# Kernel optimization log

Hardware: AMD Instinct MI355X
Metric: run time of the kernel (lower is better)

Reference implementation:

```python
import jax, jax.numpy as jnp
import numpy as np

BATCH = 16      # self.batch_size
EPS = 1e-5      # BatchNorm2d default eps


def setup_inputs() -> dict:
    key = jax.random.key(0)
    ks = jax.random.split(key, 8)
    inp = {
        # mailbox['agg_feat']: [total_nodes = B*npoints, K, C_in] = [16384, 64, 67]
        'agg_feat': jax.random.normal(ks[0], (16384, 64, 67), jnp.float32),
        # layer 0: Conv2d(67, 64, 1) + BN(64)
        'w0': jax.random.normal(ks[1], (64, 67), jnp.float32) * 0.1,
        'b0': jnp.zeros((64,), jnp.float32),
        'g0': jnp.ones((64,), jnp.float32),
        'be0': jnp.zeros((64,), jnp.float32),
        # layer 1: Conv2d(64, 64, 1) + BN(64)
        'w1': jax.random.normal(ks[2], (64, 64), jnp.float32) * 0.1,
        'b1': jnp.zeros((64,), jnp.float32),
        'g1': jnp.ones((64,), jnp.float32),
        'be1': jnp.zeros((64,), jnp.float32),
        # layer 2: Conv2d(64, 128, 1) + BN(128)
        'w2': jax.random.normal(ks[3], (128, 64), jnp.float32) * 0.1,
        'b2': jnp.zeros((128,), jnp.float32),
        'g2': jnp.ones((128,), jnp.float32),
        'be2': jnp.zeros((128,), jnp.float32),
    }
    return inp


def _conv_bn_relu(h, w, b, g, be):
    # 1x1 Conv2d on NCHW: contraction over input channels only
    h = jnp.einsum('oc,bcnk->bonk', w, h) + b[None, :, None, None]
    # BatchNorm2d in training mode: biased batch stats over (B, N, K) per channel
    mean = jnp.mean(h, axis=(0, 2, 3), keepdims=True)
    var = jnp.mean(jnp.square(h - mean), axis=(0, 2, 3), keepdims=True)
    h = (h - mean) * jax.lax.rsqrt(var + EPS)
    h = h * g[None, :, None, None] + be[None, :, None, None]
    return jax.nn.relu(h)


def reference(agg_feat, w0, b0, g0, be0, w1, b1, g1, be1, w2, b2, g2, be2):
    total, K, C = agg_feat.shape
    npoints = total // BATCH
    # [total, K, C] -> [B, npoints, K, C] -> [B, C, npoints, K]
    h = agg_feat.reshape(BATCH, npoints, K, C).transpose(0, 3, 1, 2)
    for w, b, g, be in ((w0, b0, g0, be0), (w1, b1, g1, be1), (w2, b2, g2, be2)):
        h = _conv_bn_relu(h, w, b, g, be)
    # max over neighbor axis K -> [B, C_out, npoints]
    h = jnp.max(h, axis=3)
    feat_dim = h.shape[1]
    # [B, C_out, npoints] -> [B, npoints, C_out] -> [B*npoints, C_out]
    return h.transpose(0, 2, 1).reshape(-1, feat_dim)
```

## Files before the change

kernel.cpp:

```cpp
#include <hip/hip_runtime.h>

#define ROWS  16384
#define PTOT  1048576
#define NTOTF 1048576.0f
#define EPSF  1e-5f
#define NREP  16

typedef _Float16 half8  __attribute__((ext_vector_type(8)));
typedef _Float16 half2v __attribute__((ext_vector_type(2)));
typedef __fp16   fp16x2 __attribute__((ext_vector_type(2)));
typedef __attribute__((ext_vector_type(4))) float floatx4;
typedef float f32x4 __attribute__((ext_vector_type(4)));
typedef f32x4 f32x4u __attribute__((aligned(4)));

union H8 { half8 v8; half2v v2[4]; };
union PK2 { fp16x2 p; half2v h; unsigned int u; };

__device__ __forceinline__ half2v cvt2(float lo, float hi) {
    PK2 k; k.p = __builtin_amdgcn_cvt_pkrtz(lo, hi); return k.h;
}
__device__ __forceinline__ unsigned int cvt2u(float lo, float hi) {
    PK2 k; k.p = __builtin_amdgcn_cvt_pkrtz(lo, hi); return k.u;
}
__device__ __forceinline__ float relu_f(float x) { return x > 0.f ? x : 0.f; }

__device__ __forceinline__ half8 h8zero() {
    half8 z = {(_Float16)0.f, (_Float16)0.f, (_Float16)0.f, (_Float16)0.f,
               (_Float16)0.f, (_Float16)0.f, (_Float16)0.f, (_Float16)0.f};
    return z;
}

__device__ __forceinline__ half2v bn2(half2v h, half2v a, half2v b) {
    half2v z = {(_Float16)0.f, (_Float16)0.f};
    return __builtin_elementwise_max((half2v)(h * a + b), z);
}

__global__ __launch_bounds__(256) void k_conv0(
    const float* __restrict__ X, const float* __restrict__ w0,
    const float* __restrict__ b0, _Float16* __restrict__ H,
    float* __restrict__ stats)
{
    __shared__ float sred[64], s2red[64];
    const int tid  = threadIdx.x;
    const int lane = tid & 63;
    const int wid  = tid >> 6;
    const int ln15 = lane & 15;
    const int quad = lane >> 4;
    const int pbase = blockIdx.x * 256 + wid * 64;

    if (tid < 64) { sred[tid] = 0.f; s2red[tid] = 0.f; }
    __syncthreads();

    half8 afr[4][3];
    floatx4 bias[4];
#pragma unroll
    for (int mt = 0; mt < 4; ++mt) {
        const float* wr = w0 + (size_t)(mt * 16 + ln15) * 67;
#pragma unroll
        for (int kh = 0; kh < 2; ++kh) {
            f32x4u wa = *reinterpret_cast<const f32x4u*>(wr + kh * 32 + quad * 8);
            f32x4u wb = *reinterpret_cast<const f32x4u*>(wr + kh * 32 + quad * 8 + 4);
            H8 t;
            t.v2[0] = cvt2(wa[0], wa[1]);
            t.v2[1] = cvt2(wa[2], wa[3]);
            t.v2[2] = cvt2(wb[0], wb[1]);
            t.v2[3] = cvt2(wb[2], wb[3]);
            afr[mt][kh] = t.v8;
        }
        H8 t; t.v8 = h8zero();
        if (quad == 0) {
            f32x4u tv = *reinterpret_cast<const f32x4u*>(wr + 63);
            t.v2[0] = cvt2(tv[1], tv[2]);
            t.v2[1] = cvt2(tv[3], 0.f);
        }
        afr[mt][2] = t.v8;
        bias[mt] = *reinterpret_cast<const floatx4*>(b0 + mt * 16 + quad * 4);
    }

    float s[4][4] = {}, s2[4][4] = {};
#pragma unroll 2
    for (int nt = 0; nt < 4; ++nt) {
        const int pos = pbase + nt * 16 + ln15;
        const float* xr = X + (size_t)pos * 67;
        H8 B0, B1, BT;
        {
            f32x4u xa = *reinterpret_cast<const f32x4u*>(xr + quad * 8);
            f32x4u xb = *reinterpret_cast<const f32x4u*>(xr + quad * 8 + 4);
            f32x4u xc = *reinterpret_cast<const f32x4u*>(xr + 32 + quad * 8);
            f32x4u xd = *reinterpret_cast<const f32x4u*>(xr + 32 + quad * 8 + 4);
            B0.v2[0] = cvt2(xa[0], xa[1]);
            B0.v2[1] = cvt2(xa[2], xa[3]);
            B0.v2[2] = cvt2(xb[0], xb[1]);
            B0.v2[3] = cvt2(xb[2], xb[3]);
            B1.v2[0] = cvt2(xc[0], xc[1]);
            B1.v2[1] = cvt2(xc[2], xc[3]);
            B1.v2[2] = cvt2(xd[0], xd[1]);
            B1.v2[3] = cvt2(xd[2], xd[3]);
            BT.v8 = h8zero();
            if (quad == 0) {
                f32x4u tv = *reinterpret_cast<const f32x4u*>(xr + 63);
                BT.v2[0] = cvt2(tv[1], tv[2]);
                BT.v2[1] = cvt2(tv[3], 0.f);
            }
        }
#pragma unroll
        for (int mt = 0; mt < 4; ++mt) {
            floatx4 c = bias[mt];
            c = __builtin_amdgcn_mfma_f32_16x16x32_f16(afr[mt][0], B0.v8, c, 0, 0, 0);
            c = __builtin_amdgcn_mfma_f32_16x16x32_f16(afr[mt][1], B1.v8, c, 0, 0, 0);
            c = __builtin_amdgcn_mfma_f32_16x16x32_f16(afr[mt][2], BT.v8, c, 0, 0, 0);
            s[mt][0] += c[0]; s2[mt][0] += c[0] * c[0];
            s[mt][1] += c[1]; s2[mt][1] += c[1] * c[1];
            s[mt][2] += c[2]; s2[mt][2] += c[2] * c[2];
            s[mt][3] += c[3]; s2[mt][3] += c[3] * c[3];
            uint2 o;
            o.x = cvt2u(c[0], c[1]);
            o.y = cvt2u(c[2], c[3]);
            *reinterpret_cast<uint2*>(&H[(size_t)pos * 64 + mt * 16 + quad * 4]) = o;
        }
    }
#pragma unroll
    for (int mt = 0; mt < 4; ++mt)
#pragma unroll
        for (int rg = 0; rg < 4; ++rg) {
            s[mt][rg]  += __shfl_xor(s[mt][rg], 1, 64);  s[mt][rg]  += __shfl_xor(s[mt][rg], 2, 64);
            s[mt][rg]  += __shfl_xor(s[mt][rg], 4, 64);  s[mt][rg]  += __shfl_xor(s[mt][rg], 8, 64);
            s2[mt][rg] += __shfl_xor(s2[mt][rg], 1, 64); s2[mt][rg] += __shfl_xor(s2[mt][rg], 2, 64);
            s2[mt][rg] += __shfl_xor(s2[mt][rg], 4, 64); s2[mt][rg] += __shfl_xor(s2[mt][rg], 8, 64);
        }
    if (ln15 == 0) {
#pragma unroll
        for (int mt = 0; mt < 4; ++mt)
#pragma unroll
            for (int rg = 0; rg < 4; ++rg) {
                atomicAdd(&sred[mt * 16 + quad * 4 + rg], s[mt][rg]);
                atomicAdd(&s2red[mt * 16 + quad * 4 + rg], s2[mt][rg]);
            }
    }
    __syncthreads();
    const int rep = (blockIdx.x & (NREP - 1)) * 512;
    if (tid < 64) {
        unsafeAtomicAdd(&stats[rep + tid], sred[tid]);
        unsafeAtomicAdd(&stats[rep + 64 + tid], s2red[tid]);
    }
}

__global__ __launch_bounds__(256) void k_conv1(
    const _Float16* __restrict__ Hin, _Float16* __restrict__ Hout,
    const float* __restrict__ w1, const float* __restrict__ b1,
    const float* __restrict__ g0, const float* __restrict__ be0,
    float* __restrict__ stats)
{
    __shared__ float als[64], bls[64], sred[64], s2red[64];
    const int tid  = threadIdx.x;
    const int lane = tid & 63;
    const int wid  = tid >> 6;
    const int ln15 = lane & 15;
    const int quad = lane >> 4;
    const int pbase = blockIdx.x * 256 + wid * 64;

    if (tid < 64) {
        float ssum = 0.f, qsum = 0.f;
#pragma unroll
        for (int r = 0; r < NREP; ++r) { ssum += stats[r * 512 + tid]; qsum += stats[r * 512 + 64 + tid]; }
        const float mean = ssum * (1.f / NTOTF);
        const float var  = qsum * (1.f / NTOTF) - mean * mean;
        const float a    = g0[tid] / sqrtf(var + EPSF);
        als[tid] = a; bls[tid] = be0[tid] - mean * a;
        sred[tid] = 0.f; s2red[tid] = 0.f;
    }
    __syncthreads();

    half2v a2[8], b2[8];
#pragma unroll
    for (int kh = 0; kh < 2; ++kh)
#pragma unroll
        for (int j2 = 0; j2 < 4; ++j2) {
            const int c0 = kh * 32 + quad * 8 + 2 * j2;
            half2v av = {(_Float16)als[c0], (_Float16)als[c0 + 1]};
            half2v bv = {(_Float16)bls[c0], (_Float16)bls[c0 + 1]};
            a2[kh * 4 + j2] = av; b2[kh * 4 + j2] = bv;
        }

    half8 afr[4][2];
    floatx4 bias[4];
#pragma unroll
    for (int mt = 0; mt < 4; ++mt) {
        const float* wr = w1 + (size_t)(mt * 16 + ln15) * 64;
#pragma unroll
        for (int kh = 0; kh < 2; ++kh) {
            f32x4 wa = *reinterpret_cast<const f32x4*>(wr + kh * 32 + quad * 8);
            f32x4 wb = *reinterpret_cast<const f32x4*>(wr + kh * 32 + quad * 8 + 4);
            H8 t;
            t.v2[0] = cvt2(wa[0], wa[1]);
            t.v2[1] = cvt2(wa[2], wa[3]);
            t.v2[2] = cvt2(wb[0], wb[1]);
            t.v2[3] = cvt2(wb[2], wb[3]);
            afr[mt][kh] = t.v8;
        }
        bias[mt] = *reinterpret_cast<const floatx4*>(b1 + mt * 16 + quad * 4);
    }

    float s[4][4] = {}, s2[4][4] = {};
#pragma unroll 2
    for (int nt = 0; nt < 4; ++nt) {
        const int pos = pbase + nt * 16 + ln15;
        H8 r0, r1;
        r0.v8 = *reinterpret_cast<const half8*>(&Hin[(size_t)pos * 64 + quad * 8]);
        r1.v8 = *reinterpret_cast<const half8*>(&Hin[(size_t)pos * 64 + 32 + quad * 8]);
        H8 f0, f1;
#pragma unroll
        for (int j2 = 0; j2 < 4; ++j2) {
            f0.v2[j2] = bn2(r0.v2[j2], a2[j2], b2[j2]);
            f1.v2[j2] = bn2(r1.v2[j2], a2[4 + j2], b2[4 + j2]);
        }
#pragma unroll
        for (int mt = 0; mt < 4; ++mt) {
            floatx4 c = bias[mt];
            c = __builtin_amdgcn_mfma_f32_16x16x32_f16(afr[mt][0], f0.v8, c, 0, 0, 0);
            c = __builtin_amdgcn_mfma_f32_16x16x32_f16(afr[mt][1], f1.v8, c, 0, 0, 0);
            s[mt][0] += c[0]; s2[mt][0] += c[0] * c[0];
            s[mt][1] += c[1]; s2[mt][1] += c[1] * c[1];
            s[mt][2] += c[2]; s2[mt][2] += c[2] * c[2];
            s[mt][3] += c[3]; s2[mt][3] += c[3] * c[3];
            uint2 o;
            o.x = cvt2u(c[0], c[1]);
            o.y = cvt2u(c[2], c[3]);
            *reinterpret_cast<uint2*>(&Hout[(size_t)pos * 64 + mt * 16 + quad * 4]) = o;
        }
    }
#pragma unroll
    for (int mt = 0; mt < 4; ++mt)
#pragma unroll
        for (int rg = 0; rg < 4; ++rg) {
            s[mt][rg]  += __shfl_xor(s[mt][rg], 1, 64);  s[mt][rg]  += __shfl_xor(s[mt][rg], 2, 64);
            s[mt][rg]  += __shfl_xor(s[mt][rg], 4, 64);  s[mt][rg]  += __shfl_xor(s[mt][rg], 8, 64);
            s2[mt][rg] += __shfl_xor(s2[mt][rg], 1, 64); s2[mt][rg] += __shfl_xor(s2[mt][rg], 2, 64);
            s2[mt][rg] += __shfl_xor(s2[mt][rg], 4, 64); s2[mt][rg] += __shfl_xor(s2[mt][rg], 8, 64);
        }
    if (ln15 == 0) {
#pragma unroll
        for (int mt = 0; mt < 4; ++mt)
#pragma unroll
            for (int rg = 0; rg < 4; ++rg) {
                atomicAdd(&sred[mt * 16 + quad * 4 + rg], s[mt][rg]);
                atomicAdd(&s2red[mt * 16 + quad * 4 + rg], s2[mt][rg]);
            }
    }
    __syncthreads();
    const int rep = (blockIdx.x & (NREP - 1)) * 512;
    if (tid < 64) {
        unsafeAtomicAdd(&stats[rep + 128 + tid], sred[tid]);
        unsafeAtomicAdd(&stats[rep + 192 + tid], s2red[tid]);
    }
}

__global__ __launch_bounds__(256) void k_conv2(
    const _Float16* __restrict__ H, const float* __restrict__ w2,
    const float* __restrict__ b2c, const float* __restrict__ g1,
    const float* __restrict__ be1, float* __restrict__ rowmax,
    float* __restrict__ rowmin, float* __restrict__ stats)
{
    __shared__ float als[64], bls[64], sred[128], s2red[128];
    const int tid  = threadIdx.x;
    const int lane = tid & 63;
    const int wid  = tid >> 6;
    const int ln15 = lane & 15;
    const int quad = lane >> 4;
    const int r0   = blockIdx.x * 4;

    if (tid < 64) {
        float ssum = 0.f, qsum = 0.f;
#pragma unroll
        for (int r = 0; r < NREP; ++r) { ssum += stats[r * 512 + 128 + tid]; qsum += stats[r * 512 + 192 + tid]; }
        const float mean = ssum * (1.f / NTOTF);
        const float var  = qsum * (1.f / NTOTF) - mean * mean;
        const float a    = g1[tid] / sqrtf(var + EPSF);
        als[tid] = a; bls[tid] = be1[tid] - mean * a;
    }
    if (tid < 128) { sred[tid] = 0.f; s2red[tid] = 0.f; }
    __syncthreads();

    half2v a2[8], b2[8];
#pragma unroll
    for (int kh = 0; kh < 2; ++kh)
#pragma unroll
        for (int j2 = 0; j2 < 4; ++j2) {
            const int c0 = kh * 32 + quad * 8 + 2 * j2;
            half2v av = {(_Float16)als[c0], (_Float16)als[c0 + 1]};
            half2v bv = {(_Float16)bls[c0], (_Float16)bls[c0 + 1]};
            a2[kh * 4 + j2] = av; b2[kh * 4 + j2] = bv;
        }

    const int chHalf = (wid & 1) * 64;
    half8 bfr[8];
    float biasn[4];
#pragma unroll
    for (int nt = 0; nt < 4; ++nt) {
        const int n = chHalf + nt * 16 + ln15;
        biasn[nt] = b2c[n];
#pragma unroll
        for (int kh = 0; kh < 2; ++kh) {
            f32x4 wa = *reinterpret_cast<const f32x4*>(&w2[(size_t)n * 64 + kh * 32 + quad * 8]);
            f32x4 wb = *reinterpret_cast<const f32x4*>(&w2[(size_t)n * 64 + kh * 32 + quad * 8 + 4]);
            H8 t;
            t.v2[0] = cvt2(wa[0], wa[1]);
            t.v2[1] = cvt2(wa[2], wa[3]);
            t.v2[2] = cvt2(wb[0], wb[1]);
            t.v2[3] = cvt2(wb[2], wb[3]);
            bfr[nt * 2 + kh] = t.v8;
        }
    }

    float s[4] = {0, 0, 0, 0}, s2[4] = {0, 0, 0, 0};
    for (int rr = 0; rr < 2; ++rr) {
        const int prow = r0 + (wid >> 1) * 2 + rr;
        float mx[4] = {-3.4e38f, -3.4e38f, -3.4e38f, -3.4e38f};
        float mn[4] = {3.4e38f, 3.4e38f, 3.4e38f, 3.4e38f};
#pragma unroll 2
        for (int mt = 0; mt < 4; ++mt) {
            const size_t rowb = (size_t)(prow * 64 + mt * 16 + ln15) * 64;
            H8 r0f, r1f;
            r0f.v8 = *reinterpret_cast<const half8*>(&H[rowb + quad * 8]);
            r1f.v8 = *reinterpret_cast<const half8*>(&H[rowb + 32 + quad * 8]);
            H8 f0, f1;
#pragma unroll
            for (int j2 = 0; j2 < 4; ++j2) {
                f0.v2[j2] = bn2(r0f.v2[j2], a2[j2], b2[j2]);
                f1.v2[j2] = bn2(r1f.v2[j2], a2[4 + j2], b2[4 + j2]);
            }
#pragma unroll
            for (int nt = 0; nt < 4; ++nt) {
                floatx4 a = {biasn[nt], biasn[nt], biasn[nt], biasn[nt]};
                a = __builtin_amdgcn_mfma_f32_16x16x32_f16(f0.v8, bfr[nt * 2 + 0], a, 0, 0, 0);
                a = __builtin_amdgcn_mfma_f32_16x16x32_f16(f1.v8, bfr[nt * 2 + 1], a, 0, 0, 0);
#pragma unroll
                for (int rg = 0; rg < 4; ++rg) {
                    const float h = a[rg];
                    mx[nt] = fmaxf(mx[nt], h);
                    mn[nt] = fminf(mn[nt], h);
                    s[nt] += h; s2[nt] += h * h;
                }
            }
        }
#pragma unroll
        for (int nt = 0; nt < 4; ++nt) {
            mx[nt] = fmaxf(mx[nt], __shfl_xor(mx[nt], 16, 64));
            mx[nt] = fmaxf(mx[nt], __shfl_xor(mx[nt], 32, 64));
            mn[nt] = fminf(mn[nt], __shfl_xor(mn[nt], 16, 64));
            mn[nt] = fminf(mn[nt], __shfl_xor(mn[nt], 32, 64));
        }
        if (lane < 16) {
#pragma unroll
            for (int nt = 0; nt < 4; ++nt) {
                rowmax[(size_t)prow * 128 + chHalf + nt * 16 + lane] = mx[nt];
                rowmin[(size_t)prow * 128 + chHalf + nt * 16 + lane] = mn[nt];
            }
        }
    }
#pragma unroll
    for (int nt = 0; nt < 4; ++nt) {
        s[nt]  += __shfl_xor(s[nt], 16, 64);  s[nt]  += __shfl_xor(s[nt], 32, 64);
        s2[nt] += __shfl_xor(s2[nt], 16, 64); s2[nt] += __shfl_xor(s2[nt], 32, 64);
    }
    if (lane < 16) {
#pragma unroll
        for (int nt = 0; nt < 4; ++nt) {
            atomicAdd(&sred[chHalf + nt * 16 + ln15], s[nt]);
            atomicAdd(&s2red[chHalf + nt * 16 + ln15], s2[nt]);
        }
    }
    __syncthreads();
    const int rep = (blockIdx.x & (NREP - 1)) * 512;
    if (tid < 128) {
        unsafeAtomicAdd(&stats[rep + 256 + tid], sred[tid]);
        unsafeAtomicAdd(&stats[rep + 384 + tid], s2red[tid]);
    }
}

__global__ __launch_bounds__(256) void k_out(
    const float* __restrict__ rowmax, const float* __restrict__ rowmin,
    const float* __restrict__ g2, const float* __restrict__ be2,
    const float* __restrict__ stats, float* __restrict__ out)
{
    __shared__ float als[128], bls[128];
    const int tid = threadIdx.x;
    if (tid < 128) {
        float ssum = 0.f, qsum = 0.f;
#pragma unroll
        for (int r = 0; r < NREP; ++r) { ssum += stats[r * 512 + 256 + tid]; qsum += stats[r * 512 + 384 + tid]; }
        const float mean = ssum * (1.f / NTOTF);
        const float var  = qsum * (1.f / NTOTF) - mean * mean;
        const float a    = g2[tid] / sqrtf(var + EPSF);
        als[tid] = a; bls[tid] = be2[tid] - mean * a;
    }
    __syncthreads();
    const int idx = blockIdx.x * 256 + tid;
    const int o = idx & 127;
    const float a = als[o];
    const float v = (a > 0.f) ? rowmax[idx] : rowmin[idx];
    out[idx] = relu_f(a * v + bls[o]);
}

extern "C" void kernel_launch(void* const* d_in, const int* in_sizes, int n_in,
                              void* d_out, int out_size, void* d_ws, size_t ws_size,
                              hipStream_t stream)
{
    (void)in_sizes; (void)n_in; (void)out_size; (void)ws_size;
    const float* X   = (const float*)d_in[0];
    const float* w0  = (const float*)d_in[1];
    const float* b0  = (const float*)d_in[2];
    const float* g0  = (const float*)d_in[3];
    const float* be0 = (const float*)d_in[4];
    const float* w1  = (const float*)d_in[5];
    const float* b1  = (const float*)d_in[6];
    const float* g1  = (const float*)d_in[7];
    const float* be1 = (const float*)d_in[8];
    const float* w2  = (const float*)d_in[9];
    const float* b2  = (const float*)d_in[10];
    const float* g2  = (const float*)d_in[11];
    const float* be2 = (const float*)d_in[12];
    float* out = (float*)d_out;

    char* ws = (char*)d_ws;
    _Float16* H = (_Float16*)ws;
    float* rowmax = (float*)(ws + 134217728);
    float* rowmin = (float*)(ws + 134217728 + 8388608);
    float* stats  = (float*)(ws + 134217728 + 2 * 8388608);

    hipMemsetAsync(stats, 0, NREP * 512 * sizeof(float), stream);
    hipLaunchKernelGGL(k_conv0, dim3(PTOT / 256), dim3(256), 0, stream, X, w0, b0, H, stats);
    hipLaunchKernelGGL(k_conv1, dim3(PTOT / 256), dim3(256), 0, stream, H, H, w1, b1, g0, be0, stats);
    hipLaunchKernelGGL(k_conv2, dim3(ROWS / 4), dim3(256), 0, stream, H, w2, b2, g1, be1, rowmax, rowmin, stats);
    hipLaunchKernelGGL(k_out, dim3(ROWS * 128 / 256), dim3(256), 0, stream, rowmax, rowmin, g2, be2, stats, out);
}
```

Measured before the change: 600.1 us.

## Fuse all conv/BN stages into one persistent kernel with grid barriers

Replaces the four separate launches with a single persistent kernel of 512 blocks that loops over its slice of points and uses software grid barriers (atomic counter plus flag) between the batch-norm statistics phases. The per-row max/min of the last layer stay in shared memory, and the final BN+ReLU output is written directly, so the rowmax/rowmin global round trip and the extra launches go away. In exchange, the design relies on all 512 blocks being co-resident (launch_bounds 256,2) to avoid deadlock, carries about 33KB of shared memory per block, and may lose latency hiding because each block does more serial work.

```diff
diff --git a/kernel.cpp b/kernel.cpp
--- a/kernel.cpp
+++ b/kernel.cpp
@@ -5,6 +5,7 @@
 #define NTOTF 1048576.0f
 #define EPSF  1e-5f
 #define NREP  16
+#define NBLK  512
 
 typedef _Float16 half8  __attribute__((ext_vector_type(8)));
 typedef _Float16 half2v __attribute__((ext_vector_type(2)));
@@ -35,134 +36,156 @@
     return __builtin_elementwise_max((half2v)(h * a + b), z);
 }
 
-__global__ __launch_bounds__(256) void k_conv0(
-    const float* __restrict__ X, const float* __restrict__ w0,
-    const float* __restrict__ b0, _Float16* __restrict__ H,
-    float* __restrict__ stats)
+__device__ __forceinline__ float aload(const float* p) {
+    return __hip_atomic_load(p, __ATOMIC_RELAXED, __HIP_MEMORY_SCOPE_AGENT);
+}
+
+__device__ __forceinline__ void gridbar(unsigned int* cnt, unsigned int* flg) {
+    __syncthreads();
+    if (threadIdx.x == 0) {
+        __threadfence();
+        if (atomicAdd(cnt, 1u) == NBLK - 1u) {
+            __threadfence();
+            __hip_atomic_store(flg, 1u, __ATOMIC_RELEASE, __HIP_MEMORY_SCOPE_AGENT);
+        } else {
+            while (__hip_atomic_load(flg, __ATOMIC_ACQUIRE, __HIP_MEMORY_SCOPE_AGENT) == 0u)
+                __builtin_amdgcn_s_sleep(8);
+        }
+    }
+    __syncthreads();
+}
+
+__global__ __launch_bounds__(256, 2) void k_fused(
+    const float* __restrict__ X,
+    const float* __restrict__ w0, const float* __restrict__ b0,
+    const float* __restrict__ g0, const float* __restrict__ be0,
+    const float* __restrict__ w1, const float* __restrict__ b1,
+    const float* __restrict__ g1, const float* __restrict__ be1,
+    const float* __restrict__ w2, const float* __restrict__ cb2,
+    const float* __restrict__ g2, const float* __restrict__ be2,
+    const _Float16* __restrict__ Hin, _Float16* __restrict__ Hout,
+    float* __restrict__ stats, unsigned int* __restrict__ bar,
+    float* __restrict__ out)
 {
-    __shared__ float sred[64], s2red[64];
+    __shared__ float als[128], bls[128], sred[128], s2red[128];
+    __shared__ float smx[32 * 128], smn[32 * 128];
+
     const int tid  = threadIdx.x;
     const int lane = tid & 63;
     const int wid  = tid >> 6;
     const int ln15 = lane & 15;
     const int quad = lane >> 4;
-    const int pbase = blockIdx.x * 256 + wid * 64;
+    const int blk  = blockIdx.x;
+    const int rep  = (blk & (NREP - 1)) * 512;
 
     if (tid < 64) { sred[tid] = 0.f; s2red[tid] = 0.f; }
     __syncthreads();
 
-    half8 afr[4][3];
-    floatx4 bias[4];
-#pragma unroll
-    for (int mt = 0; mt < 4; ++mt) {
-        const float* wr = w0 + (size_t)(mt * 16 + ln15) * 67;
-#pragma unroll
-        for (int kh = 0; kh < 2; ++kh) {
-            f32x4u wa = *reinterpret_cast<const f32x4u*>(wr + kh * 32 + quad * 8);
-            f32x4u wb = *reinterpret_cast<const f32x4u*>(wr + kh * 32 + quad * 8 + 4);
-            H8 t;
-            t.v2[0] = cvt2(wa[0], wa[1]);
-            t.v2[1] = cvt2(wa[2], wa[3]);
-            t.v2[2] = cvt2(wb[0], wb[1]);
-            t.v2[3] = cvt2(wb[2], wb[3]);
-            afr[mt][kh] = t.v8;
-        }
-        H8 t; t.v8 = h8zero();
-        if (quad == 0) {
-            f32x4u tv = *reinterpret_cast<const f32x4u*>(wr + 63);
-            t.v2[0] = cvt2(tv[1], tv[2]);
-            t.v2[1] = cvt2(tv[3], 0.f);
-        }
-        afr[mt][2] = t.v8;
-        bias[mt] = *reinterpret_cast<const floatx4*>(b0 + mt * 16 + quad * 4);
-    }
-
-    float s[4][4] = {}, s2[4][4] = {};
+    {
+        half8 afr[4][3];
+        floatx4 bias[4];
+#pragma unroll
+        for (int mt = 0; mt < 4; ++mt) {
+            const float* wr = w0 + (size_t)(mt * 16 + ln15) * 67;
+#pragma unroll
+            for (int kh = 0; kh < 2; ++kh) {
+                f32x4u wa = *reinterpret_cast<const f32x4u*>(wr + kh * 32 + quad * 8);
+                f32x4u wb = *reinterpret_cast<const f32x4u*>(wr + kh * 32 + quad * 8 + 4);
+                H8 t;
+                t.v2[0] = cvt2(wa[0], wa[1]);
+                t.v2[1] = cvt2(wa[2], wa[3]);
+                t.v2[2] = cvt2(wb[0], wb[1]);
+                t.v2[3] = cvt2(wb[2], wb[3]);
+                afr[mt][kh] = t.v8;
+            }
+            H8 t; t.v8 = h8zero();
+            if (quad == 0) {
+                f32x4u tv = *reinterpret_cast<const f32x4u*>(wr + 63);
+                t.v2[0] = cvt2(tv[1], tv[2]);
+                t.v2[1] = cvt2(tv[3], 0.f);
+            }
+            afr[mt][2] = t.v8;
+            bias[mt] = *reinterpret_cast<const floatx4*>(b0 + mt * 16 + quad * 4);
+        }
+
+        float s[4][4] = {}, s2[4][4] = {};
+        for (int it = 0; it < 8; ++it) {
+            const int pbase = blk * 2048 + it * 256 + wid * 64;
 #pragma unroll 2
-    for (int nt = 0; nt < 4; ++nt) {
-        const int pos = pbase + nt * 16 + ln15;
-        const float* xr = X + (size_t)pos * 67;
-        H8 B0, B1, BT;
-        {
-            f32x4u xa = *reinterpret_cast<const f32x4u*>(xr + quad * 8);
-            f32x4u xb = *reinterpret_cast<const f32x4u*>(xr + quad * 8 + 4);
-            f32x4u xc = *reinterpret_cast<const f32x4u*>(xr + 32 + quad * 8);
-            f32x4u xd = *reinterpret_cast<const f32x4u*>(xr + 32 + quad * 8 + 4);
-            B0.v2[0] = cvt2(xa[0], xa[1]);
-            B0.v2[1] = cvt2(xa[2], xa[3]);
-            B0.v2[2] = cvt2(xb[0], xb[1]);
-            B0.v2[3] = cvt2(xb[2], xb[3]);
-            B1.v2[0] = cvt2(xc[0], xc[1]);
-            B1.v2[1] = cvt2(xc[2], xc[3]);
-            B1.v2[2] = cvt2(xd[0], xd[1]);
-            B1.v2[3] = cvt2(xd[2], xd[3]);
-            BT.v8 = h8zero();
-            if (quad == 0) {
-                f32x4u tv = *reinterpret_cast<const f32x4u*>(xr + 63);
-                BT.v2[0] = cvt2(tv[1], tv[2]);
-                BT.v2[1] = cvt2(tv[3], 0.f);
-            }
-        }
-#pragma unroll
-        for (int mt = 0; mt < 4; ++mt) {
-            floatx4 c = bias[mt];
-            c = __builtin_amdgcn_mfma_f32_16x16x32_f16(afr[mt][0], B0.v8, c, 0, 0, 0);
-            c = __builtin_amdgcn_mfma_f32_16x16x32_f16(afr[mt][1], B1.v8, c, 0, 0, 0);
-            c = __builtin_amdgcn_mfma_f32_16x16x32_f16(afr[mt][2], BT.v8, c, 0, 0, 0);
-            s[mt][0] += c[0]; s2[mt][0] += c[0] * c[0];
-            s[mt][1] += c[1]; s2[mt][1] += c[1] * c[1];
-            s[mt][2] += c[2]; s2[mt][2] += c[2] * c[2];
-            s[mt][3] += c[3]; s2[mt][3] += c[3] * c[3];
-            uint2 o;
-            o.x = cvt2u(c[0], c[1]);
-            o.y = cvt2u(c[2], c[3]);
-            *reinterpret_cast<uint2*>(&H[(size_t)pos * 64 + mt * 16 + quad * 4]) = o;
-        }
-    }
-#pragma unroll
-    for (int mt = 0; mt < 4; ++mt)
-#pragma unroll
-        for (int rg = 0; rg < 4; ++rg) {
-            s[mt][rg]  += __shfl_xor(s[mt][rg], 1, 64);  s[mt][rg]  += __shfl_xor(s[mt][rg], 2, 64);
-            s[mt][rg]  += __shfl_xor(s[mt][rg], 4, 64);  s[mt][rg]  += __shfl_xor(s[mt][rg], 8, 64);
-            s2[mt][rg] += __shfl_xor(s2[mt][rg], 1, 64); s2[mt][rg] += __shfl_xor(s2[mt][rg], 2, 64);
-            s2[mt][rg] += __shfl_xor(s2[mt][rg], 4, 64); s2[mt][rg] += __shfl_xor(s2[mt][rg], 8, 64);
-        }
-    if (ln15 == 0) {
+            for (int nt = 0; nt < 4; ++nt) {
+                const int pos = pbase + nt * 16 + ln15;
+                const float* xr = X + (size_t)pos * 67;
+                H8 B0, B1, BT;
+                {
+                    f32x4u xa = *reinterpret_cast<const f32x4u*>(xr + quad * 8);
+                    f32x4u xb = *reinterpret_cast<const f32x4u*>(xr + quad * 8 + 4);
+                    f32x4u xc = *reinterpret_cast<const f32x4u*>(xr + 32 + quad * 8);
+                    f32x4u xd = *reinterpret_cast<const f32x4u*>(xr + 32 + quad * 8 + 4);
+                    B0.v2[0] = cvt2(xa[0], xa[1]);
+                    B0.v2[1] = cvt2(xa[2], xa[3]);
+                    B0.v2[2] = cvt2(xb[0], xb[1]);
+                    B0.v2[3] = cvt2(xb[2], xb[3]);
+                    B1.v2[0] = cvt2(xc[0], xc[1]);
+                    B1.v2[1] = cvt2(xc[2], xc[3]);
+                    B1.v2[2] = cvt2(xd[0], xd[1]);
+                    B1.v2[3] = cvt2(xd[2], xd[3]);
+                    BT.v8 = h8zero();
+                    if (quad == 0) {
+                        f32x4u tv = *reinterpret_cast<const f32x4u*>(xr + 63);
+                        BT.v2[0] = cvt2(tv[1], tv[2]);
+                        BT.v2[1] = cvt2(tv[3], 0.f);
+                    }
+                }
+#pragma unroll
+                for (int mt = 0; mt < 4; ++mt) {
+                    floatx4 c = bias[mt];
+                    c = __builtin_amdgcn_mfma_f32_16x16x32_f16(afr[mt][0], B0.v8, c, 0, 0, 0);
+                    c = __builtin_amdgcn_mfma_f32_16x16x32_f16(afr[mt][1], B1.v8, c, 0, 0, 0);
+                    c = __builtin_amdgcn_mfma_f32_16x16x32_f16(afr[mt][2], BT.v8, c, 0, 0, 0);
+                    s[mt][0] += c[0]; s2[mt][0] += c[0] * c[0];
+                    s[mt][1] += c[1]; s2[mt][1] += c[1] * c[1];
+                    s[mt][2] += c[2]; s2[mt][2] += c[2] * c[2];
+                    s[mt][3] += c[3]; s2[mt][3] += c[3] * c[3];
+                    uint2 o;
+                    o.x = cvt2u(c[0], c[1]);
+                    o.y = cvt2u(c[2], c[3]);
+                    *reinterpret_cast<uint2*>(&Hout[(size_t)pos * 64 + mt * 16 + quad * 4]) = o;
+                }
+            }
+        }
 #pragma unroll
         for (int mt = 0; mt < 4; ++mt)
 #pragma unroll
             for (int rg = 0; rg < 4; ++rg) {
-                atomicAdd(&sred[mt * 16 + quad * 4 + rg], s[mt][rg]);
-                atomicAdd(&s2red[mt * 16 + quad * 4 + rg], s2[mt][rg]);
-            }
-    }
-    __syncthreads();
-    const int rep = (blockIdx.x & (NREP - 1)) * 512;
-    if (tid < 64) {
-        unsafeAtomicAdd(&stats[rep + tid], sred[tid]);
-        unsafeAtomicAdd(&stats[rep + 64 + tid], s2red[tid]);
-    }
-}
-
-__global__ __launch_bounds__(256) void k_conv1(
-    const _Float16* __restrict__ Hin, _Float16* __restrict__ Hout,
-    const float* __restrict__ w1, const float* __restrict__ b1,
-    const float* __restrict__ g0, const float* __restrict__ be0,
-    float* __restrict__ stats)
-{
-    __shared__ float als[64], bls[64], sred[64], s2red[64];
-    const int tid  = threadIdx.x;
-    const int lane = tid & 63;
-    const int wid  = tid >> 6;
-    const int ln15 = lane & 15;
-    const int quad = lane >> 4;
-    const int pbase = blockIdx.x * 256 + wid * 64;
+                s[mt][rg]  += __shfl_xor(s[mt][rg], 1, 64);  s[mt][rg]  += __shfl_xor(s[mt][rg], 2, 64);
+                s[mt][rg]  += __shfl_xor(s[mt][rg], 4, 64);  s[mt][rg]  += __shfl_xor(s[mt][rg], 8, 64);
+                s2[mt][rg] += __shfl_xor(s2[mt][rg], 1, 64); s2[mt][rg] += __shfl_xor(s2[mt][rg], 2, 64);
+                s2[mt][rg] += __shfl_xor(s2[mt][rg], 4, 64); s2[mt][rg] += __shfl_xor(s2[mt][rg], 8, 64);
+            }
+        if (ln15 == 0) {
+#pragma unroll
+            for (int mt = 0; mt < 4; ++mt)
+#pragma unroll
+                for (int rg = 0; rg < 4; ++rg) {
+                    atomicAdd(&sred[mt * 16 + quad * 4 + rg], s[mt][rg]);
+                    atomicAdd(&s2red[mt * 16 + quad * 4 + rg], s2[mt][rg]);
+                }
+        }
+        __syncthreads();
+        if (tid < 64) {
+            unsafeAtomicAdd(&stats[rep + tid], sred[tid]);
+            unsafeAtomicAdd(&stats[rep + 64 + tid], s2red[tid]);
+        }
+    }
+    gridbar(&bar[0], &bar[1]);
 
     if (tid < 64) {
         float ssum = 0.f, qsum = 0.f;
 #pragma unroll
-        for (int r = 0; r < NREP; ++r) { ssum += stats[r * 512 + tid]; qsum += stats[r * 512 + 64 + tid]; }
+        for (int r = 0; r < NREP; ++r) {
+            ssum += aload(&stats[r * 512 + tid]);
+            qsum += aload(&stats[r * 512 + 64 + tid]);
+        }
         const float mean = ssum * (1.f / NTOTF);
         const float var  = qsum * (1.f / NTOTF) - mean * mean;
         const float a    = g0[tid] / sqrtf(var + EPSF);
@@ -171,108 +194,101 @@
     }
     __syncthreads();
 
-    half2v a2[8], b2[8];
-#pragma unroll
-    for (int kh = 0; kh < 2; ++kh)
-#pragma unroll
-        for (int j2 = 0; j2 < 4; ++j2) {
-            const int c0 = kh * 32 + quad * 8 + 2 * j2;
-            half2v av = {(_Float16)als[c0], (_Float16)als[c0 + 1]};
-            half2v bv = {(_Float16)bls[c0], (_Float16)bls[c0 + 1]};
-            a2[kh * 4 + j2] = av; b2[kh * 4 + j2] = bv;
-        }
-
-    half8 afr[4][2];
-    floatx4 bias[4];
-#pragma unroll
-    for (int mt = 0; mt < 4; ++mt) {
-        const float* wr = w1 + (size_t)(mt * 16 + ln15) * 64;
-#pragma unroll
-        for (int kh = 0; kh < 2; ++kh) {
-            f32x4 wa = *reinterpret_cast<const f32x4*>(wr + kh * 32 + quad * 8);
-            f32x4 wb = *reinterpret_cast<const f32x4*>(wr + kh * 32 + quad * 8 + 4);
-            H8 t;
-            t.v2[0] = cvt2(wa[0], wa[1]);
-            t.v2[1] = cvt2(wa[2], wa[3]);
-            t.v2[2] = cvt2(wb[0], wb[1]);
-            t.v2[3] = cvt2(wb[2], wb[3]);
-            afr[mt][kh] = t.v8;
-        }
-        bias[mt] = *reinterpret_cast<const floatx4*>(b1 + mt * 16 + quad * 4);
-    }
-
-    float s[4][4] = {}, s2[4][4] = {};
+    {
+        half2v ba2[8], bb2[8];
+#pragma unroll
+        for (int kh = 0; kh < 2; ++kh)
+#pragma unroll
+            for (int j2 = 0; j2 < 4; ++j2) {
+                const int c0 = kh * 32 + quad * 8 + 2 * j2;
+                half2v av = {(_Float16)als[c0], (_Float16)als[c0 + 1]};
+                half2v bv = {(_Float16)bls[c0], (_Float16)bls[c0 + 1]};
+                ba2[kh * 4 + j2] = av; bb2[kh * 4 + j2] = bv;
+            }
+
+        half8 afr[4][2];
+        floatx4 bias[4];
+#pragma unroll
+        for (int mt = 0; mt < 4; ++mt) {
+            const float* wr = w1 + (size_t)(mt * 16 + ln15) * 64;
+#pragma unroll
+            for (int kh = 0; kh < 2; ++kh) {
+                f32x4 wa = *reinterpret_cast<const f32x4*>(wr + kh * 32 + quad * 8);
+                f32x4 wb = *reinterpret_cast<const f32x4*>(wr + kh * 32 + quad * 8 + 4);
+                H8 t;
+                t.v2[0] = cvt2(wa[0], wa[1]);
+                t.v2[1] = cvt2(wa[2], wa[3]);
+                t.v2[2] = cvt2(wb[0], wb[1]);
+                t.v2[3] = cvt2(wb[2], wb[3]);
+                afr[mt][kh] = t.v8;
+            }
+            bias[mt] = *reinterpret_cast<const floatx4*>(b1 + mt * 16 + quad * 4);
+        }
+
+        float s[4][4] = {}, s2[4][4] = {};
+        for (int it = 0; it < 8; ++it) {
+            const int pbase = blk * 2048 + it * 256 + wid * 64;
 #pragma unroll 2
-    for (int nt = 0; nt < 4; ++nt) {
-        const int pos = pbase + nt * 16 + ln15;
-        H8 r0, r1;
-        r0.v8 = *reinterpret_cast<const half8*>(&Hin[(size_t)pos * 64 + quad * 8]);
-        r1.v8 = *reinterpret_cast<const half8*>(&Hin[(size_t)pos * 64 + 32 + quad * 8]);
-        H8 f0, f1;
-#pragma unroll
-        for (int j2 = 0; j2 < 4; ++j2) {
-            f0.v2[j2] = bn2(r0.v2[j2], a2[j2], b2[j2]);
-            f1.v2[j2] = bn2(r1.v2[j2], a2[4 + j2], b2[4 + j2]);
-        }
-#pragma unroll
-        for (int mt = 0; mt < 4; ++mt) {
-            floatx4 c = bias[mt];
-            c = __builtin_amdgcn_mfma_f32_16x16x32_f16(afr[mt][0], f0.v8, c, 0, 0, 0);
-            c = __builtin_amdgcn_mfma_f32_16x16x32_f16(afr[mt][1], f1.v8, c, 0, 0, 0);
-            s[mt][0] += c[0]; s2[mt][0] += c[0] * c[0];
-            s[mt][1] += c[1]; s2[mt][1] += c[1] * c[1];
-            s[mt][2] += c[2]; s2[mt][2] += c[2] * c[2];
-            s[mt][3] += c[3]; s2[mt][3] += c[3] * c[3];
-            uint2 o;
-            o.x = cvt2u(c[0], c[1]);
-            o.y = cvt2u(c[2], c[3]);
-            *reinterpret_cast<uint2*>(&Hout[(size_t)pos * 64 + mt * 16 + quad * 4]) = o;
-        }
-    }
-#pragma unroll
-    for (int mt = 0; mt < 4; ++mt)
-#pragma unroll
-        for (int rg = 0; rg < 4; ++rg) {
-            s[mt][rg]  += __shfl_xor(s[mt][rg], 1, 64);  s[mt][rg]  += __shfl_xor(s[mt][rg], 2, 64);
-            s[mt][rg]  += __shfl_xor(s[mt][rg], 4, 64);  s[mt][rg]  += __shfl_xor(s[mt][rg], 8, 64);
-            s2[mt][rg] += __shfl_xor(s2[mt][rg], 1, 64); s2[mt][rg] += __shfl_xor(s2[mt][rg], 2, 64);
-            s2[mt][rg] += __shfl_xor(s2[mt][rg], 4, 64); s2[mt][rg] += __shfl_xor(s2[mt][rg], 8, 64);
-        }
-    if (ln15 == 0) {
+            for (int nt = 0; nt < 4; ++nt) {
+                const int pos = pbase + nt * 16 + ln15;
+                H8 r0, r1;
+                r0.v8 = *reinterpret_cast<const half8*>(&Hin[(size_t)pos * 64 + quad * 8]);
+                r1.v8 = *reinterpret_cast<const half8*>(&Hin[(size_t)pos * 64 + 32 + quad * 8]);
+                H8 f0, f1;
+#pragma unroll
+                for (int j2 = 0; j2 < 4; ++j2) {
+                    f0.v2[j2] = bn2(r0.v2[j2], ba2[j2], bb2[j2]);
+                    f1.v2[j2] = bn2(r1.v2[j2], ba2[4 + j2], bb2[4 + j2]);
+                }
+#pragma unroll
+                for (int mt = 0; mt < 4; ++mt) {
+                    floatx4 c = bias[mt];
+                    c = __builtin_amdgcn_mfma_f32_16x16x32_f16(afr[mt][0], f0.v8, c, 0, 0, 0);
+                    c = __builtin_amdgcn_mfma_f32_16x16x32_f16(afr[mt][1], f1.v8, c, 0, 0, 0);
+                    s[mt][0] += c[0]; s2[mt][0] += c[0] * c[0];
+                    s[mt][1] += c[1]; s2[mt][1] += c[1] * c[1];
+                    s[mt][2] += c[2]; s2[mt][2] += c[2] * c[2];
+                    s[mt][3] += c[3]; s2[mt][3] += c[3] * c[3];
+                    uint2 o;
+                    o.x = cvt2u(c[0], c[1]);
+                    o.y = cvt2u(c[2], c[3]);
+                    *reinterpret_cast<uint2*>(&Hout[(size_t)pos * 64 + mt * 16 + quad * 4]) = o;
+                }
+            }
+        }
 #pragma unroll
         for (int mt = 0; mt < 4; ++mt)
 #pragma unroll
             for (int rg = 0; rg < 4; ++rg) {
-                atomicAdd(&sred[mt * 16 + quad * 4 + rg], s[mt][rg]);
-                atomicAdd(&s2red[mt * 16 + quad * 4 + rg], s2[mt][rg]);
-            }
-    }
-    __syncthreads();
-    const int rep = (blockIdx.x & (NREP - 1)) * 512;
-    if (tid < 64) {
-        unsafeAtomicAdd(&stats[rep + 128 + tid], sred[tid]);
-        unsafeAtomicAdd(&stats[rep + 192 + tid], s2red[tid]);
-    }
-}
-
-__global__ __launch_bounds__(256) void k_conv2(
-    const _Float16* __restrict__ H, const float* __restrict__ w2,
-    const float* __restrict__ b2c, const float* __restrict__ g1,
-    const float* __restrict__ be1, float* __restrict__ rowmax,
-    float* __restrict__ rowmin, float* __restrict__ stats)
-{
-    __shared__ float als[64], bls[64], sred[128], s2red[128];
-    const int tid  = threadIdx.x;
-    const int lane = tid & 63;
-    const int wid  = tid >> 6;
-    const int ln15 = lane & 15;
-    const int quad = lane >> 4;
-    const int r0   = blockIdx.x * 4;
+                s[mt][rg]  += __shfl_xor(s[mt][rg], 1, 64);  s[mt][rg]  += __shfl_xor(s[mt][rg], 2, 64);
+                s[mt][rg]  += __shfl_xor(s[mt][rg], 4, 64);  s[mt][rg]  += __shfl_xor(s[mt][rg], 8, 64);
+                s2[mt][rg] += __shfl_xor(s2[mt][rg], 1, 64); s2[mt][rg] += __shfl_xor(s2[mt][rg], 2, 64);
+                s2[mt][rg] += __shfl_xor(s2[mt][rg], 4, 64); s2[mt][rg] += __shfl_xor(s2[mt][rg], 8, 64);
+            }
+        if (ln15 == 0) {
+#pragma unroll
+            for (int mt = 0; mt < 4; ++mt)
+#pragma unroll
+                for (int rg = 0; rg < 4; ++rg) {
+                    atomicAdd(&sred[mt * 16 + quad * 4 + rg], s[mt][rg]);
+                    atomicAdd(&s2red[mt * 16 + quad * 4 + rg], s2[mt][rg]);
+                }
+        }
+        __syncthreads();
+        if (tid < 64) {
+            unsafeAtomicAdd(&stats[rep + 128 + tid], sred[tid]);
+            unsafeAtomicAdd(&stats[rep + 192 + tid], s2red[tid]);
+        }
+    }
+    gridbar(&bar[2], &bar[3]);
 
     if (tid < 64) {
         float ssum = 0.f, qsum = 0.f;
 #pragma unroll
-        for (int r = 0; r < NREP; ++r) { ssum += stats[r * 512 + 128 + tid]; qsum += stats[r * 512 + 192 + tid]; }
+        for (int r = 0; r < NREP; ++r) {
+            ssum += aload(&stats[r * 512 + 128 + tid]);
+            qsum += aload(&stats[r * 512 + 192 + tid]);
+        }
         const float mean = ssum * (1.f / NTOTF);
         const float var  = qsum * (1.f / NTOTF) - mean * mean;
         const float a    = g1[tid] / sqrtf(var + EPSF);
@@ -281,125 +297,129 @@
     if (tid < 128) { sred[tid] = 0.f; s2red[tid] = 0.f; }
     __syncthreads();
 
-    half2v a2[8], b2[8];
-#pragma unroll
-    for (int kh = 0; kh < 2; ++kh)
-#pragma unroll
-        for (int j2 = 0; j2 < 4; ++j2) {
-            const int c0 = kh * 32 + quad * 8 + 2 * j2;
-            half2v av = {(_Float16)als[c0], (_Float16)als[c0 + 1]};
-            half2v bv = {(_Float16)bls[c0], (_Float16)bls[c0 + 1]};
-            a2[kh * 4 + j2] = av; b2[kh * 4 + j2] = bv;
-        }
-
-    const int chHalf = (wid & 1) * 64;
-    half8 bfr[8];
-    float biasn[4];
-#pragma unroll
-    for (int nt = 0; nt < 4; ++nt) {
-        const int n = chHalf + nt * 16 + ln15;
-        biasn[nt] = b2c[n];
-#pragma unroll
-        for (int kh = 0; kh < 2; ++kh) {
-            f32x4 wa = *reinterpret_cast<const f32x4*>(&w2[(size_t)n * 64 + kh * 32 + quad * 8]);
-            f32x4 wb = *reinterpret_cast<const f32x4*>(&w2[(size_t)n * 64 + kh * 32 + quad * 8 + 4]);
-            H8 t;
-            t.v2[0] = cvt2(wa[0], wa[1]);
-            t.v2[1] = cvt2(wa[2], wa[3]);
-            t.v2[2] = cvt2(wb[0], wb[1]);
-            t.v2[3] = cvt2(wb[2], wb[3]);
-            bfr[nt * 2 + kh] = t.v8;
-        }
-    }
-
-    float s[4] = {0, 0, 0, 0}, s2[4] = {0, 0, 0, 0};
-    for (int rr = 0; rr < 2; ++rr) {
-        const int prow = r0 + (wid >> 1) * 2 + rr;
-        float mx[4] = {-3.4e38f, -3.4e38f, -3.4e38f, -3.4e38f};
-        float mn[4] = {3.4e38f, 3.4e38f, 3.4e38f, 3.4e38f};
+    {
+        half2v ba2[8], bb2[8];
+#pragma unroll
+        for (int kh = 0; kh < 2; ++kh)
+#pragma unroll
+            for (int j2 = 0; j2 < 4; ++j2) {
+                const int c0 = kh * 32 + quad * 8 + 2 * j2;
+                half2v av = {(_Float16)als[c0], (_Float16)als[c0 + 1]};
+                half2v bv = {(_Float16)bls[c0], (_Float16)bls[c0 + 1]};
+                ba2[kh * 4 + j2] = av; bb2[kh * 4 + j2] = bv;
+            }
+
+        const int chHalf = (wid & 1) * 64;
+        half8 bfr[8];
+        float biasn[4];
+#pragma unroll
+        for (int nt = 0; nt < 4; ++nt) {
+            const int n = chHalf + nt * 16 + ln15;
+            biasn[nt] = cb2[n];
+#pragma unroll
+            for (int kh = 0; kh < 2; ++kh) {
+                f32x4 wa = *reinterpret_cast<const f32x4*>(&w2[(size_t)n * 64 + kh * 32 + quad * 8]);
+                f32x4 wb = *reinterpret_cast<const f32x4*>(&w2[(size_t)n * 64 + kh * 32 + quad * 8 + 4]);
+                H8 t;
+                t.v2[0] = cvt2(wa[0], wa[1]);
+                t.v2[1] = cvt2(wa[2], wa[3]);
+                t.v2[2] = cvt2(wb[0], wb[1]);
+                t.v2[3] = cvt2(wb[2], wb[3]);
+                bfr[nt * 2 + kh] = t.v8;
+            }
+        }
+
+        float s[4] = {0, 0, 0, 0}, s2[4] = {0, 0, 0, 0};
+        for (int it = 0; it < 8; ++it) {
+            for (int rr = 0; rr < 2; ++rr) {
+                const int rl   = it * 4 + (wid >> 1) * 2 + rr;
+                const int prow = blk * 32 + rl;
+                float mx[4] = {-3.4e38f, -3.4e38f, -3.4e38f, -3.4e38f};
+                float mn[4] = {3.4e38f, 3.4e38f, 3.4e38f, 3.4e38f};
 #pragma unroll 2
-        for (int mt = 0; mt < 4; ++mt) {
-            const size_t rowb = (size_t)(prow * 64 + mt * 16 + ln15) * 64;
-            H8 r0f, r1f;
-            r0f.v8 = *reinterpret_cast<const half8*>(&H[rowb + quad * 8]);
-            r1f.v8 = *reinterpret_cast<const half8*>(&H[rowb + 32 + quad * 8]);
-            H8 f0, f1;
-#pragma unroll
-            for (int j2 = 0; j2 < 4; ++j2) {
-                f0.v2[j2] = bn2(r0f.v2[j2], a2[j2], b2[j2]);
-                f1.v2[j2] = bn2(r1f.v2[j2], a2[4 + j2], b2[4 + j2]);
-            }
+                for (int mt = 0; mt < 4; ++mt) {
+                    const size_t rowb = (size_t)(prow * 64 + mt * 16 + ln15) * 64;
+                    H8 r0f, r1f;
+                    r0f.v8 = *reinterpret_cast<const half8*>(&Hin[rowb + quad * 8]);
+                    r1f.v8 = *reinterpret_cast<const half8*>(&Hin[rowb + 32 + quad * 8]);
+                    H8 f0, f1;
+#pragma unroll
+                    for (int j2 = 0; j2 < 4; ++j2) {
+                        f0.v2[j2] = bn2(r0f.v2[j2], ba2[j2], bb2[j2]);
+                        f1.v2[j2] = bn2(r1f.v2[j2], ba2[4 + j2], bb2[4 + j2]);
+                    }
+#pragma unroll
+                    for (int nt = 0; nt < 4; ++nt) {
+                        floatx4 a = {biasn[nt], biasn[nt], biasn[nt], biasn[nt]};
+                        a = __builtin_amdgcn_mfma_f32_16x16x32_f16(f0.v8, bfr[nt * 2 + 0], a, 0, 0, 0);
+                        a = __builtin_amdgcn_mfma_f32_16x16x32_f16(f1.v8, bfr[nt * 2 + 1], a, 0, 0, 0);
+#pragma unroll
+                        for (int rg = 0; rg < 4; ++rg) {
+                            const float h = a[rg];
+                            mx[nt] = fmaxf(mx[nt], h);
+                            mn[nt] = fminf(mn[nt], h);
+                            s[nt] += h; s2[nt] += h * h;
+                        }
+                    }
+                }
+#pragma unroll
+                for (int nt = 0; nt < 4; ++nt) {
+                    mx[nt] = fmaxf(mx[nt], __shfl_xor(mx[nt], 16, 64));
+                    mx[nt] = fmaxf(mx[nt], __shfl_xor(mx[nt], 32, 64));
+                    mn[nt] = fminf(mn[nt], __shfl_xor(mn[nt], 16, 64));
+                    mn[nt] = fminf(mn[nt], __shfl_xor(mn[nt], 32, 64));
+                }
+                if (lane < 16) {
+#pragma unroll
+                    for (int nt = 0; nt < 4; ++nt) {
+                        smx[rl * 128 + chHalf + nt * 16 + lane] = mx[nt];
+                        smn[rl * 128 + chHalf + nt * 16 + lane] = mn[nt];
+                    }
+                }
+            }
+        }
+#pragma unroll
+        for (int nt = 0; nt < 4; ++nt) {
+            s[nt]  += __shfl_xor(s[nt], 16, 64);  s[nt]  += __shfl_xor(s[nt], 32, 64);
+            s2[nt] += __shfl_xor(s2[nt], 16, 64); s2[nt] += __shfl_xor(s2[nt], 32, 64);
+        }
+        if (lane < 16) {
 #pragma unroll
             for (int nt = 0; nt < 4; ++nt) {
-                floatx4 a = {biasn[nt], biasn[nt], biasn[nt], biasn[nt]};
-                a = __builtin_amdgcn_mfma_f32_16x16x32_f16(f0.v8, bfr[nt * 2 + 0], a, 0, 0, 0);
-                a = __builtin_amdgcn_mfma_f32_16x16x32_f16(f1.v8, bfr[nt * 2 + 1], a, 0, 0, 0);
-#pragma unroll
-                for (int rg = 0; rg < 4; ++rg) {
-                    const float h = a[rg];
-                    mx[nt] = fmaxf(mx[nt], h);
-                    mn[nt] = fminf(mn[nt], h);
-                    s[nt] += h; s2[nt] += h * h;
-                }
-            }
-        }
-#pragma unroll
-        for (int nt = 0; nt < 4; ++nt) {
-            mx[nt] = fmaxf(mx[nt], __shfl_xor(mx[nt], 16, 64));
-            mx[nt] = fmaxf(mx[nt], __shfl_xor(mx[nt], 32, 64));
-            mn[nt] = fminf(mn[nt], __shfl_xor(mn[nt], 16, 64));
-            mn[nt] = fminf(mn[nt], __shfl_xor(mn[nt], 32, 64));
-        }
-        if (lane < 16) {
-#pragma unroll
-            for (int nt = 0; nt < 4; ++nt) {
-                rowmax[(size_t)prow * 128 + chHalf + nt * 16 + lane] = mx[nt];
-                rowmin[(size_t)prow * 128 + chHalf + nt * 16 + lane] = mn[nt];
-            }
-        }
-    }
-#pragma unroll
-    for (int nt = 0; nt < 4; ++nt) {
-        s[nt]  += __shfl_xor(s[nt], 16, 64);  s[nt]  += __shfl_xor(s[nt], 32, 64);
-        s2[nt] += __shfl_xor(s2[nt], 16, 64); s2[nt] += __shfl_xor(s2[nt], 32, 64);
-    }
-    if (lane < 16) {
-#pragma unroll
-        for (int nt = 0; nt < 4; ++nt) {
-            atomicAdd(&sred[chHalf + nt * 16 + ln15], s[nt]);
-            atomicAdd(&s2red[chHalf + nt * 16 + ln15], s2[nt]);
-        }
-    }
-    __syncthreads();
-    const int rep = (blockIdx.x & (NREP - 1)) * 512;
-    if (tid < 128) {
-        unsafeAtomicAdd(&stats[rep + 256 + tid], sred[tid]);
-        unsafeAtomicAdd(&stats[rep + 384 + tid], s2red[tid]);
-    }
-}
-
-__global__ __launch_bounds__(256) void k_out(
-    const float* __restrict__ rowmax, const float* __restrict__ rowmin,
-    const float* __restrict__ g2, const float* __restrict__ be2,
-    const float* __restrict__ stats, float* __restrict__ out)
-{
-    __shared__ float als[128], bls[128];
-    const int tid = threadIdx.x;
+                atomicAdd(&sred[chHalf + nt * 16 + ln15], s[nt]);
+                atomicAdd(&s2red[chHalf + nt * 16 + ln15], s2[nt]);
+            }
+        }
+        __syncthreads();
+        if (tid < 128) {
+            unsafeAtomicAdd(&stats[rep + 256 + tid], sred[tid]);
+            unsafeAtomicAdd(&stats[rep + 384 + tid], s2red[tid]);
+        }
+    }
+    gridbar(&bar[4], &bar[5]);
+
     if (tid < 128) {
         float ssum = 0.f, qsum = 0.f;
 #pragma unroll
-        for (int r = 0; r < NREP; ++r) { ssum += stats[r * 512 + 256 + tid]; qsum += stats[r * 512 + 384 + tid]; }
+        for (int r = 0; r < NREP; ++r) {
+            ssum += aload(&stats[r * 512 + 256 + tid]);
+            qsum += aload(&stats[r * 512 + 384 + tid]);
+        }
         const float mean = ssum * (1.f / NTOTF);
         const float var  = qsum * (1.f / NTOTF) - mean * mean;
         const float a    = g2[tid] / sqrtf(var + EPSF);
         als[tid] = a; bls[tid] = be2[tid] - mean * a;
     }
     __syncthreads();
-    const int idx = blockIdx.x * 256 + tid;
-    const int o = idx & 127;
-    const float a = als[o];
-    const float v = (a > 0.f) ? rowmax[idx] : rowmin[idx];
-    out[idx] = relu_f(a * v + bls[o]);
+
+#pragma unroll
+    for (int j = 0; j < 16; ++j) {
+        const int local = j * 256 + tid;
+        const int ch = local & 127;
+        const float a = als[ch];
+        const float v = (a > 0.f) ? smx[local] : smn[local];
+        out[(size_t)blk * 4096 + local] = relu_f(a * v + bls[ch]);
+    }
 }
 
 extern "C" void kernel_launch(void* const* d_in, const int* in_sizes, int n_in,
@@ -424,13 +444,11 @@
 
     char* ws = (char*)d_ws;
     _Float16* H = (_Float16*)ws;
-    float* rowmax = (float*)(ws + 134217728);
-    float* rowmin = (float*)(ws + 134217728 + 8388608);
-    float* stats  = (float*)(ws + 134217728 + 2 * 8388608);
-
-    hipMemsetAsync(stats, 0, NREP * 512 * sizeof(float), stream);
-    hipLaunchKernelGGL(k_conv0, dim3(PTOT / 256), dim3(256), 0, stream, X, w0, b0, H, stats);
-    hipLaunchKernelGGL(k_conv1, dim3(PTOT / 256), dim3(256), 0, stream, H, H, w1, b1, g0, be0, stats);
-    hipLaunchKernelGGL(k_conv2, dim3(ROWS / 4), dim3(256), 0, stream, H, w2, b2, g1, be1, rowmax, rowmin, stats);
-    hipLaunchKernelGGL(k_out, dim3(ROWS * 128 / 256), dim3(256), 0, stream, rowmax, rowmin, g2, be2, stats, out);
-}
+    float* stats = (float*)(ws + 134217728);
+    unsigned int* bar = (unsigned int*)(stats + NREP * 512);
+
+    hipMemsetAsync(stats, 0, (NREP * 512 + 16) * sizeof(float), stream);
+    hipLaunchKernelGGL(k_fused, dim3(NBLK), dim3(256), 0, stream,
+                       X, w0, b0, g0, be0, w1, b1, g1, be1, w2, b2, g2, be2,
+                       H, H, stats, bar, out);
+}
```

Result: slower. 831.5 us (+38.6%).
